# Optimization experiments

Measured on AMD Instinct MI355X. Metric: run time of the kernel, lower is better.

The kernel has to match this reference:

```python
import jax, jax.numpy as jnp
import numpy as np

N = 100_000      # nodes
E = 1_600_000    # edges (avg degree 16)
D = 128          # emb_dim
L = 2            # num_layer
BN_EPS = 1e-5


def setup_inputs() -> dict:
    key = jax.random.key(0)
    ks = jax.random.split(key, 16)
    s = 0.05
    inp = {
        # int inputs
        "x": jax.random.randint(ks[0], (N, 9), 0, 2),
        "z": jax.random.randint(ks[1], (N,), 0, 1000),
        "edge_index": jax.random.randint(ks[2], (2, E), 0, N),
        "edge_attr": jax.random.randint(ks[3], (E, 3), 0, 2),
        # learned params
        "atom_emb": jax.random.normal(ks[4], (9, 119, D), jnp.float32) * s,  # padded stacked AtomEncoder tables
        "z_emb": jax.random.normal(ks[5], (1000, D), jnp.float32) * s,
        "bond_emb": jax.random.normal(ks[6], (L, 3, 6, D), jnp.float32) * s,  # padded BondEncoder tables per layer
        "eps": jnp.zeros((L,), jnp.float32),
        "W1": jax.random.normal(ks[7], (L, D, 2 * D), jnp.float32) * s,
        "b1": jnp.zeros((L, 2 * D), jnp.float32),
        "g1": jnp.ones((L, 2 * D), jnp.float32),
        "be1": jnp.zeros((L, 2 * D), jnp.float32),
        "W2": jax.random.normal(ks[8], (L, 2 * D, D), jnp.float32) * s,
        "b2": jnp.zeros((L, D), jnp.float32),
        "bng": jnp.ones((L, D), jnp.float32),
        "bnb": jnp.zeros((L, D), jnp.float32),
    }
    return inp


def _batchnorm(h, g, b):
    # training-mode BatchNorm1d: batch stats, biased variance
    m = h.mean(axis=0)
    v = h.var(axis=0)
    return (h - m) * jax.lax.rsqrt(v + BN_EPS) * g + b


def _multi_embed(tables, idx):
    # tables: [F, V, D], idx: [N, F] -> sum_f tables[f][idx[:, f]]  -> [N, D]
    return jax.vmap(lambda t, i: t[i], in_axes=(0, 1))(tables, idx).sum(axis=0)


def reference(x, z, edge_index, edge_attr, atom_emb, z_emb, bond_emb, eps,
              W1, b1, g1, be1, W2, b2, bng, bnb):
    src, dst = edge_index[0], edge_index[1]
    # h0 = AtomEncoder(x) + z_embedding(z)
    h = _multi_embed(atom_emb, x) + z_emb[z]
    for l in range(L):
        # GINConv: bond encode -> gather -> relu message -> scatter-add -> MLP
        e_emb = _multi_embed(bond_emb[l], edge_attr)          # [E, D]
        msg = jax.nn.relu(h[src] + e_emb)                      # [E, D]
        agg = jax.ops.segment_sum(msg, dst, num_segments=N)    # [N, D]
        pre = (1.0 + eps[l]) * h + agg
        hid = jax.nn.relu(_batchnorm(pre @ W1[l] + b1[l], g1[l], be1[l]))
        hconv = hid @ W2[l] + b2[l]
        h = _batchnorm(hconv, bng[l], bnb[l])
        if l < L - 1:
            h = jax.nn.relu(h)   # dropout ratio 0 -> identity
    return h
```

## Files before the change

### kernel.cpp

```cpp
#include <hip/hip_runtime.h>

#define D 128
#define BN_EPS 1e-5f
#define NSUB 1024
#define CAP2 2048

typedef __attribute__((ext_vector_type(8))) short short8;
typedef __attribute__((ext_vector_type(4))) float floatx4;

__device__ __forceinline__ float bf2f(unsigned short u) {
    unsigned int x = ((unsigned int)u) << 16;
    return __builtin_bit_cast(float, x);
}
__device__ __forceinline__ unsigned short f2bf(float f) {
    unsigned int x = __builtin_bit_cast(unsigned int, f);
    x = x + 0x7FFFu + ((x >> 16) & 1u);
    return (unsigned short)(x >> 16);
}
__device__ __forceinline__ int magdiv(unsigned int x, unsigned long long magic) {
    return (int)(((unsigned long long)x * magic) >> 44);
}

__global__ __launch_bounds__(256)
void setup_kernel(const int* __restrict__ x, const int* __restrict__ z,
                  const float* __restrict__ atom_emb, const float* __restrict__ z_emb,
                  unsigned short* __restrict__ hb, int N, int nbNode,
                  const float* __restrict__ bond_emb, unsigned short* __restrict__ comb,
                  const float* __restrict__ W1, unsigned short* __restrict__ w1p,
                  const float* __restrict__ W2, unsigned short* __restrict__ w2p) {
    const int b = blockIdx.x;
    const int tid = threadIdx.x;
    if (b < nbNode) {
        int gid = b * 256 + tid;
        int node = gid >> 5;
        if (node >= N) return;
        int d0 = (gid & 31) * 4;
        float4 acc = *(const float4*)(z_emb + (size_t)z[node] * D + d0);
#pragma unroll
        for (int f = 0; f < 9; ++f) {
            int v = x[node * 9 + f];
            const float4 t = *(const float4*)(atom_emb + (size_t)(f * 119 + v) * D + d0);
            acc.x += t.x; acc.y += t.y; acc.z += t.z; acc.w += t.w;
        }
        ushort4 o;
        o.x = f2bf(acc.x); o.y = f2bf(acc.y); o.z = f2bf(acc.z); o.w = f2bf(acc.w);
        *(ushort4*)(hb + (size_t)node * D + d0) = o;
    } else if (b < nbNode + 216) {
        int t = (b - nbNode) * 256 + tid;
        int layer = t / (216 * D);
        int idx = t - layer * (216 * D);
        int c = idx >> 7, d = idx & 127;
        int a0 = c / 36, a1 = (c / 6) % 6, a2 = c % 6;
        const float* bb = bond_emb + (size_t)layer * 3 * 6 * D;
        float v = bb[(0 * 6 + a0) * D + d] + bb[(1 * 6 + a1) * D + d] + bb[(2 * 6 + a2) * D + d];
        comb[(size_t)layer * 216 * D + idx] = f2bf(v);
    } else {
        int isW2 = (b >= nbNode + 216 + 256);
        int t = (b - nbNode - 216 - (isW2 ? 256 : 0)) * 256 + tid;
        int layer = t >> 15;
        int idx = t & 32767;
        int logN = isW2 ? 7 : 8;
        int NCOLS = 1 << logN;
        int k = idx >> logN, n = idx & (NCOLS - 1);
        int k0 = k >> 5, kq = k & 31, q = kq >> 3, j = kq & 7;
        int tt = n >> 4, ln = n & 15;
        size_t dest = (((size_t)k0 * (NCOLS >> 4) + tt) << 9) + ((q << 4) + ln) * 8 + j;
        const float* W = (isW2 ? W2 : W1) + (size_t)layer * 32768;
        unsigned short* Wp = (isW2 ? w2p : w1p) + (size_t)layer * 32768;
        Wp[dest] = f2bf(W[idx]);
    }
}

__global__ __launch_bounds__(256)
void partition1_kernel(const int* __restrict__ ei, const int* __restrict__ ea,
                       int2* __restrict__ l1, int* __restrict__ tail1,
                       int E, unsigned long long magic, int capE, int ntiles, int nblocks) {
    __shared__ int lcnt[4][8], lbase[4][8];
    const int tid = threadIdx.x;
    const int wid = tid >> 6;
    for (int tile = blockIdx.x; tile < ntiles; tile += nblocks) {
        const int tb = tile * 4096;
        if (tid < 32) ((int*)lcnt)[tid] = 0;
        __syncthreads();
        int mydst[16], mypay[16];
#pragma unroll
        for (int j = 0; j < 16; ++j) {
            int e = tb + j * 256 + tid;
            if (e < E) {
                int dst = ei[E + e];
                int c = (ea[3 * e] * 6 + ea[3 * e + 1]) * 6 + ea[3 * e + 2];
                mydst[j] = dst;
                mypay[j] = ei[e] | (c << 17);
                atomicAdd(&lcnt[wid][magdiv((unsigned)dst * 8u, magic)], 1);
            } else {
                mydst[j] = -1;
            }
        }
        __syncthreads();
        if (tid < 32) {
            int w = tid >> 3, s = tid & 7;
            lbase[w][s] = atomicAdd(&tail1[s], lcnt[w][s]);
            lcnt[w][s] = 0;
        }
        __syncthreads();
#pragma unroll
        for (int j = 0; j < 16; ++j) {
            if (mydst[j] >= 0) {
                int s = magdiv((unsigned)mydst[j] * 8u, magic);
                int pos = lbase[wid][s] + atomicAdd(&lcnt[wid][s], 1);
                if (pos < capE) l1[(size_t)s * capE + pos] = make_int2(mydst[j], mypay[j]);
            }
        }
        __syncthreads();
    }
}

__global__ __launch_bounds__(256)
void partition2_kernel(const int2* __restrict__ l1, const int* __restrict__ tail1,
                       unsigned int* __restrict__ subL, int* __restrict__ tail2,
                       int N, unsigned long long magic, int capE, int G) {
    __shared__ int lcnt[128], lbase[128];
    const int s = blockIdx.x & 7;
    const int g = blockIdx.x >> 3;
    const int tid = threadIdx.x;
    const int len = min(tail1[s], capE);
    const int2* src = l1 + (size_t)s * capE;
    for (int tb = g * 4096; tb < len; tb += G * 4096) {
        if (tid < 128) lcnt[tid] = 0;
        __syncthreads();
        int2 e[16];
        int sub[16];
#pragma unroll
        for (int j = 0; j < 16; ++j) {
            int i = tb + j * 256 + tid;
            if (i < len) {
                e[j] = src[i];
                sub[j] = magdiv((unsigned)e[j].x * 1024u, magic) - (s << 7);
                atomicAdd(&lcnt[sub[j]], 1);
            } else {
                sub[j] = -1;
            }
        }
        __syncthreads();
        if (tid < 128) {
            lbase[tid] = atomicAdd(&tail2[(s << 7) + tid], lcnt[tid]);
            lcnt[tid] = 0;
        }
        __syncthreads();
#pragma unroll
        for (int j = 0; j < 16; ++j) {
            if (sub[j] >= 0) {
                int k = (s << 7) + sub[j];
                int lo = (int)(((long long)k * N + 1023) >> 10);
                int pos = lbase[sub[j]] + atomicAdd(&lcnt[sub[j]], 1);
                if (pos < CAP2)
                    subL[(size_t)k * CAP2 + pos] =
                        (unsigned int)e[j].y | ((unsigned int)(e[j].x - lo) << 25);
            }
        }
        __syncthreads();
    }
}

__global__ __launch_bounds__(1024)
void subscan_kernel(const int* __restrict__ tail2, int* __restrict__ subbase,
                    int* __restrict__ offsets, int N) {
    const int tid = threadIdx.x, lane = tid & 63, wid = tid >> 6;
    int v = min(tail2[tid], CAP2);
    int s = v;
#pragma unroll
    for (int off = 1; off < 64; off <<= 1) {
        int t = __shfl_up(s, off, 64);
        if (lane >= off) s += t;
    }
    __shared__ int ws[16];
    if (lane == 63) ws[wid] = s;
    __syncthreads();
    if (wid == 0) {
        int w = (lane < 16) ? ws[lane] : 0;
#pragma unroll
        for (int off = 1; off < 16; off <<= 1) {
            int t = __shfl_up(w, off, 64);
            if (lane >= off) w += t;
        }
        if (lane < 16) ws[lane] = w;
    }
    __syncthreads();
    int excl = (wid ? ws[wid - 1] : 0) + s - v;
    subbase[tid] = excl;
    if (tid == 1023) offsets[N] = excl + v;
}

__global__ __launch_bounds__(256)
void csr_sort_kernel(const unsigned int* __restrict__ subL, const int* __restrict__ tail2,
                     const int* __restrict__ subbase, int* __restrict__ offsets,
                     int* __restrict__ bucket, int N) {
    const int k = blockIdx.x;
    const int tid = threadIdx.x, lane = tid & 63, wid = tid >> 6;
    const int len = min(tail2[k], CAP2);
    const int base = subbase[k];
    const int lo = (int)(((long long)k * N + 1023) >> 10);
    const int hi = (int)(((long long)(k + 1) * N + 1023) >> 10);
    const int nn = hi - lo;
    __shared__ int cnt[128], loff[128], wsum[4];
    __shared__ unsigned int sorted[CAP2];
    const unsigned int* src = subL + (size_t)k * CAP2;

    if (tid < 128) cnt[tid] = 0;
    __syncthreads();
    for (int i = tid; i < len; i += 256) atomicAdd(&cnt[src[i] >> 25], 1);
    __syncthreads();
    int v = (tid < 128) ? cnt[tid] : 0;
    int s = v;
#pragma unroll
    for (int off = 1; off < 64; off <<= 1) {
        int t = __shfl_up(s, off, 64);
        if (lane >= off) s += t;
    }
    if (lane == 63) wsum[wid] = s;
    __syncthreads();
    if (tid < 128) loff[tid] = ((wid == 1) ? wsum[0] : 0) + s - v;
    __syncthreads();
    if (tid < nn) offsets[lo + tid] = base + loff[tid];
    if (tid < 128) cnt[tid] = 0;
    __syncthreads();
    for (int i = tid; i < len; i += 256) {
        unsigned int e = src[i];
        int ld = e >> 25;
        int pos = loff[ld] + atomicAdd(&cnt[ld], 1);
        sorted[pos] = e & 0x1FFFFFFu;
    }
    __syncthreads();
    for (int i = tid; i < len; i += 256) bucket[base + i] = (int)sorted[i];
}

__global__ __launch_bounds__(256)
void gather_reduce_kernel(const int* __restrict__ offsets, const int* __restrict__ bucket,
                          const unsigned short* __restrict__ comb,
                          const unsigned short* __restrict__ hb,
                          const float* __restrict__ eps_l,
                          unsigned short* __restrict__ pre, int N) {
    int gid = blockIdx.x * blockDim.x + threadIdx.x;
    int node = gid >> 4;
    if (node >= N) return;
    int d0 = (gid & 15) * 8;

    union U8 { int4 i; unsigned short u[8]; };
    float s = 1.0f + eps_l[0];
    float a[8];
    {
        U8 hv; hv.i = *(const int4*)(hb + (size_t)node * D + d0);
#pragma unroll
        for (int j = 0; j < 8; ++j) a[j] = bf2f(hv.u[j]) * s;
    }
    const int beg = offsets[node], end = offsets[node + 1];
    for (int p = beg; p < end; p += 4) {
        int rem = end - p;
        int pk0 = bucket[p];
        int pk1 = bucket[rem > 1 ? p + 1 : p];
        int pk2 = bucket[rem > 2 ? p + 2 : p];
        int pk3 = bucket[rem > 3 ? p + 3 : p];
        U8 h0, h1, h2, h3, c0, c1, c2, c3;
        h0.i = *(const int4*)(hb + (size_t)(pk0 & 0x1FFFF) * D + d0);
        c0.i = *(const int4*)(comb + (size_t)((pk0 >> 17) & 0xFF) * D + d0);
        h1.i = *(const int4*)(hb + (size_t)(pk1 & 0x1FFFF) * D + d0);
        c1.i = *(const int4*)(comb + (size_t)((pk1 >> 17) & 0xFF) * D + d0);
        h2.i = *(const int4*)(hb + (size_t)(pk2 & 0x1FFFF) * D + d0);
        c2.i = *(const int4*)(comb + (size_t)((pk2 >> 17) & 0xFF) * D + d0);
        h3.i = *(const int4*)(hb + (size_t)(pk3 & 0x1FFFF) * D + d0);
        c3.i = *(const int4*)(comb + (size_t)((pk3 >> 17) & 0xFF) * D + d0);
#pragma unroll
        for (int j = 0; j < 8; ++j) a[j] += fmaxf(bf2f(h0.u[j]) + bf2f(c0.u[j]), 0.0f);
        if (rem > 1) {
#pragma unroll
            for (int j = 0; j < 8; ++j) a[j] += fmaxf(bf2f(h1.u[j]) + bf2f(c1.u[j]), 0.0f);
        }
        if (rem > 2) {
#pragma unroll
            for (int j = 0; j < 8; ++j) a[j] += fmaxf(bf2f(h2.u[j]) + bf2f(c2.u[j]), 0.0f);
        }
        if (rem > 3) {
#pragma unroll
            for (int j = 0; j < 8; ++j) a[j] += fmaxf(bf2f(h3.u[j]) + bf2f(c3.u[j]), 0.0f);
        }
    }
    U8 o;
#pragma unroll
    for (int j = 0; j < 8; ++j) o.u[j] = f2bf(a[j]);
    *(int4*)(pre + (size_t)node * D + d0) = o.i;
}

template <int K, int NCOLS, int TRANSFORM, int OUTBF>
__global__ __launch_bounds__(256)
void mfma_gemm_kernel(const unsigned short* __restrict__ A,
                      const unsigned short* __restrict__ Wp,
                      const float* __restrict__ bias,
                      const float* __restrict__ tscale, const float* __restrict__ tshift,
                      unsigned short* __restrict__ Cbf, float* __restrict__ Cf,
                      float* __restrict__ partial, int M) {
    constexpr int NT = NCOLS / 16;
    constexpr int NCHUNK = K / 32;
    constexpr int CPP = NCHUNK / 2;
    __shared__ unsigned short Ws[16384];
    __shared__ float red[NCOLS * 2];

    const int tid = threadIdx.x;
    const int wave = tid >> 6, lane = tid & 63;
    const int quad = lane >> 4, ln = lane & 15;
    const int m_base = blockIdx.x * 64 + wave * 16;
    int arow = m_base + ln;
    if (arow >= M) arow = M - 1;
    const int kq = quad * 8;

    int4 araw[NCHUNK];
#pragma unroll
    for (int c = 0; c < NCHUNK; ++c)
        araw[c] = *(const int4*)(A + (size_t)arow * K + c * 32 + kq);

    for (int i = tid; i < NCOLS * 2; i += 256) red[i] = 0.f;

    floatx4 acc[NT];
#pragma unroll
    for (int t = 0; t < NT; ++t) acc[t] = (floatx4){0.f, 0.f, 0.f, 0.f};

#pragma unroll
    for (int ph = 0; ph < 2; ++ph) {
        if (ph) __syncthreads();
#pragma unroll
        for (int i = 0; i < 16384; i += 2048)
            *(int4*)&Ws[i + tid * 8] = *(const int4*)&Wp[ph * 16384 + i + tid * 8];
        __syncthreads();
#pragma unroll
        for (int cc = 0; cc < CPP; ++cc) {
            const int c = ph * CPP + cc;
            short8 afrag;
            if constexpr (TRANSFORM) {
                union { int4 i; unsigned short u[8]; } raw;
                raw.i = araw[c];
                const int kb = c * 32 + kq;
                float4 sc0 = *(const float4*)(tscale + kb);
                float4 sc1 = *(const float4*)(tscale + kb + 4);
                float4 sh0 = *(const float4*)(tshift + kb);
                float4 sh1 = *(const float4*)(tshift + kb + 4);
                union { short8 v; unsigned short u[8]; } au;
                au.u[0] = f2bf(fmaxf(bf2f(raw.u[0]) * sc0.x + sh0.x, 0.f));
                au.u[1] = f2bf(fmaxf(bf2f(raw.u[1]) * sc0.y + sh0.y, 0.f));
                au.u[2] = f2bf(fmaxf(bf2f(raw.u[2]) * sc0.z + sh0.z, 0.f));
                au.u[3] = f2bf(fmaxf(bf2f(raw.u[3]) * sc0.w + sh0.w, 0.f));
                au.u[4] = f2bf(fmaxf(bf2f(raw.u[4]) * sc1.x + sh1.x, 0.f));
                au.u[5] = f2bf(fmaxf(bf2f(raw.u[5]) * sc1.y + sh1.y, 0.f));
                au.u[6] = f2bf(fmaxf(bf2f(raw.u[6]) * sc1.z + sh1.z, 0.f));
                au.u[7] = f2bf(fmaxf(bf2f(raw.u[7]) * sc1.w + sh1.w, 0.f));
                afrag = au.v;
            } else {
                afrag = __builtin_bit_cast(short8, araw[c]);
            }
#pragma unroll
            for (int t = 0; t < NT; ++t) {
                short8 bfrag = *(const short8*)&Ws[(((cc * NT) + t) << 9) + lane * 8];
                acc[t] = __builtin_amdgcn_mfma_f32_16x16x32_bf16(afrag, bfrag, acc[t], 0, 0, 0);
            }
        }
    }

#pragma unroll
    for (int t = 0; t < NT; ++t) {
        int col = t * 16 + ln;
        float bv = bias[col];
        float sv = 0.f, qv = 0.f;
#pragma unroll
        for (int r = 0; r < 4; ++r) {
            int row = m_base + quad * 4 + r;
            if (row < M) {
                float v = acc[t][r] + bv;
                sv += v; qv += v * v;
                if constexpr (OUTBF) Cbf[(size_t)row * NCOLS + col] = f2bf(v);
                else                 Cf[(size_t)row * NCOLS + col] = v;
            }
        }
        sv += __shfl_xor(sv, 16, 64); sv += __shfl_xor(sv, 32, 64);
        qv += __shfl_xor(qv, 16, 64); qv += __shfl_xor(qv, 32, 64);
        if (quad == 0) {
            atomicAdd(&red[col], sv);
            atomicAdd(&red[NCOLS + col], qv);
        }
    }
    __syncthreads();
    float* pout = partial + (size_t)blockIdx.x * (NCOLS * 2);
    for (int i = tid; i < NCOLS * 2; i += 256) pout[i] = red[i];
}

template <int NCOLS>
__global__ __launch_bounds__(256)
void reduce_stats_kernel(const float* __restrict__ partial, int nb,
                         const float* __restrict__ g, const float* __restrict__ b,
                         float* __restrict__ scale, float* __restrict__ shift, float invN) {
    const int col = blockIdx.x;
    const int tid = threadIdx.x;
    float s = 0.f, q = 0.f;
    for (int bb = tid; bb < nb; bb += 256) {
        const float* p = partial + (size_t)bb * (NCOLS * 2);
        s += p[col];
        q += p[NCOLS + col];
    }
#pragma unroll
    for (int off = 32; off > 0; off >>= 1) {
        s += __shfl_xor(s, off, 64);
        q += __shfl_xor(q, off, 64);
    }
    __shared__ float ws[4], wq[4];
    if ((tid & 63) == 0) { ws[tid >> 6] = s; wq[tid >> 6] = q; }
    __syncthreads();
    if (tid == 0) {
        s = ws[0] + ws[1] + ws[2] + ws[3];
        q = wq[0] + wq[1] + wq[2] + wq[3];
        float mean = s * invN;
        float var = q * invN - mean * mean;
        float inv = 1.0f / sqrtf(var + BN_EPS);
        float sc = g[col] * inv;
        scale[col] = sc;
        shift[col] = b[col] - mean * sc;
    }
}

__global__ void bn_apply_kernel(const float* __restrict__ Xf, const unsigned short* __restrict__ Xb,
                                float* __restrict__ Yf, unsigned short* __restrict__ Yb,
                                const float* __restrict__ scale, const float* __restrict__ shift,
                                int N, int mode) {
    int gid = blockIdx.x * blockDim.x + threadIdx.x;
    int node = gid >> 5;
    if (node >= N) return;
    int d0 = (gid & 31) * 4;
    float4 v;
    if (mode == 0) {
        ushort4 b = *(const ushort4*)(Xb + (size_t)node * D + d0);
        v.x = bf2f(b.x); v.y = bf2f(b.y); v.z = bf2f(b.z); v.w = bf2f(b.w);
    } else {
        v = *(const float4*)(Xf + (size_t)node * D + d0);
    }
    float4 sc = *(const float4*)(scale + d0);
    float4 sh = *(const float4*)(shift + d0);
    float4 o;
    o.x = v.x * sc.x + sh.x;
    o.y = v.y * sc.y + sh.y;
    o.z = v.z * sc.z + sh.z;
    o.w = v.w * sc.w + sh.w;
    if (mode == 0) {
        ushort4 ob;
        ob.x = f2bf(fmaxf(o.x, 0.f));
        ob.y = f2bf(fmaxf(o.y, 0.f));
        ob.z = f2bf(fmaxf(o.z, 0.f));
        ob.w = f2bf(fmaxf(o.w, 0.f));
        *(ushort4*)(Yb + (size_t)node * D + d0) = ob;
    } else {
        *(float4*)(Yf + (size_t)node * D + d0) = o;
    }
}

extern "C" void kernel_launch(void* const* d_in, const int* in_sizes, int n_in,
                              void* d_out, int out_size, void* d_ws, size_t ws_size,
                              hipStream_t stream) {
    const int*   x        = (const int*)d_in[0];
    const int*   z        = (const int*)d_in[1];
    const int*   ei       = (const int*)d_in[2];
    const int*   ea       = (const int*)d_in[3];
    const float* atom_emb = (const float*)d_in[4];
    const float* z_emb    = (const float*)d_in[5];
    const float* bond_emb = (const float*)d_in[6];
    const float* eps      = (const float*)d_in[7];
    const float* W1       = (const float*)d_in[8];
    const float* b1       = (const float*)d_in[9];
    const float* g1       = (const float*)d_in[10];
    const float* be1      = (const float*)d_in[11];
    const float* W2       = (const float*)d_in[12];
    const float* b2       = (const float*)d_in[13];
    const float* bng      = (const float*)d_in[14];
    const float* bnb      = (const float*)d_in[15];

    const int N = in_sizes[1];
    const int E = in_sizes[3] / 3;

    float* h = (float*)d_out;

    const int ngb = (N + 63) / 64;
    const int capE = E / 8 + E / 64;
    const unsigned long long magic = ((1ULL << 44) / (unsigned int)N) + 1;

    char* ws = (char*)d_ws;
    size_t off = 0;
    auto alloc = [&](size_t bytes) { void* p = ws + off; off += (bytes + 255) & ~(size_t)255; return p; };
    unsigned short* pre_bf = (unsigned short*)alloc((size_t)N * D * 2);
    unsigned short* extra  = (unsigned short*)alloc((size_t)N * D * 2);
    (void)extra;
    float* out2 = (float*)pre_bf;
    unsigned short* out2_bf = pre_bf;
    unsigned short* out1_bf = (unsigned short*)alloc((size_t)N * 2 * D * 2);
    unsigned short* hb      = (unsigned short*)alloc((size_t)N * D * 2);
    int* offsets = (int*)alloc((size_t)(N + 1) * 4);
    int* bucket  = (int*)alloc((size_t)E * 4);
    int2* l1     = (int2*)alloc((size_t)8 * capE * 8);
    unsigned int* subL = (unsigned int*)alloc((size_t)NSUB * CAP2 * 4);
    int* subbase = (int*)alloc(NSUB * 4);
    float* stats = (float*)alloc(1024 * 4);
    float* partial1 = (float*)alloc((size_t)ngb * 512 * 4);
    float* partial2 = (float*)alloc((size_t)ngb * 256 * 4);
    unsigned short* w1p  = (unsigned short*)alloc((size_t)2 * D * 2 * D * 2);
    unsigned short* w2p  = (unsigned short*)alloc((size_t)2 * 2 * D * D * 2);
    unsigned short* comb = (unsigned short*)alloc((size_t)2 * 216 * D * 2);
    int* tail1 = (int*)out1_bf;
    int* tail2 = tail1 + 8;

    float* scale1 = stats;
    float* shift1 = stats + 256;
    float* scale2 = stats + 512;
    float* shift2 = stats + 640;

    const float invN = 1.0f / (float)N;
    const int ntiles = (E + 4095) / 4096;
    const int nbNode = (N * 32 + 255) / 256;

    hipMemsetAsync(tail1, 0, (8 + NSUB) * sizeof(int), stream);
    partition1_kernel<<<256, 256, 0, stream>>>(ei, ea, l1, tail1, E, magic, capE, ntiles, 256);
    partition2_kernel<<<256, 256, 0, stream>>>(l1, tail1, subL, tail2, N, magic, capE, 32);
    subscan_kernel<<<1, 1024, 0, stream>>>(tail2, subbase, offsets, N);
    csr_sort_kernel<<<NSUB, 256, 0, stream>>>(subL, tail2, subbase, offsets, bucket, N);

    setup_kernel<<<nbNode + 216 + 256 + 256, 256, 0, stream>>>(
        x, z, atom_emb, z_emb, hb, N, nbNode, bond_emb, comb, W1, w1p, W2, w2p);

    for (int l = 0; l < 2; ++l) {
        gather_reduce_kernel<<<(N * 16 + 255) / 256, 256, 0, stream>>>(
            offsets, bucket, comb + (size_t)l * 216 * D, hb, eps + l, pre_bf, N);

        mfma_gemm_kernel<128, 256, 0, 1><<<ngb, 256, 0, stream>>>(
            pre_bf, w1p + (size_t)l * D * 2 * D, b1 + (size_t)l * 2 * D,
            nullptr, nullptr, out1_bf, nullptr, partial1, N);
        reduce_stats_kernel<256><<<256, 256, 0, stream>>>(
            partial1, ngb, g1 + (size_t)l * 2 * D, be1 + (size_t)l * 2 * D,
            scale1, shift1, invN);

        if (l == 0) {
            mfma_gemm_kernel<256, 128, 1, 1><<<ngb, 256, 0, stream>>>(
                out1_bf, w2p + (size_t)l * 2 * D * D, b2 + (size_t)l * D,
                scale1, shift1, out2_bf, nullptr, partial2, N);
        } else {
            mfma_gemm_kernel<256, 128, 1, 0><<<ngb, 256, 0, stream>>>(
                out1_bf, w2p + (size_t)l * 2 * D * D, b2 + (size_t)l * D,
                scale1, shift1, nullptr, out2, partial2, N);
        }
        reduce_stats_kernel<128><<<128, 256, 0, stream>>>(
            partial2, ngb, bng + (size_t)l * D, bnb + (size_t)l * D,
            scale2, shift2, invN);

        bn_apply_kernel<<<(N * 32 + 255) / 256, 256, 0, stream>>>(
            out2, out2_bf, h, hb, scale2, shift2, N, l == 0 ? 0 : 1);
    }
}
```

Baseline: 574.7 us.

## Merge partition passes, widen gather to 64 lanes per node, drop fp32 output path

The two-stage edge partition becomes a single pass that bins edges straight into 1024 sub-buckets using shared counters, removing the intermediate l1 buffer and one kernel launch. The gather-reduce now gives each node a full 64-lane wavefront, with four edge groups in parallel and a shuffle reduction, so per-node latency on the irregular gathers shrinks. The last layer's second GEMM now writes bf16 instead of fp32 before BN apply, which cuts traffic but costs some output precision. Shared-memory atomics on 1024 counters may contend more, and idle lanes on low-degree nodes are a risk.

```diff
diff --git a/kernel.cpp b/kernel.cpp
--- a/kernel.cpp
+++ b/kernel.cpp
@@ -72,90 +72,49 @@
 }
 
 __global__ __launch_bounds__(256)
-void partition1_kernel(const int* __restrict__ ei, const int* __restrict__ ea,
-                       int2* __restrict__ l1, int* __restrict__ tail1,
-                       int E, unsigned long long magic, int capE, int ntiles, int nblocks) {
-    __shared__ int lcnt[4][8], lbase[4][8];
+void partition_kernel(const int* __restrict__ ei, const int* __restrict__ ea,
+                      unsigned int* __restrict__ subL, int* __restrict__ tail2,
+                      int E, int N, unsigned long long magic, int ntiles, int nblocks) {
+    __shared__ int lcnt[1024], lbase[1024];
     const int tid = threadIdx.x;
-    const int wid = tid >> 6;
     for (int tile = blockIdx.x; tile < ntiles; tile += nblocks) {
         const int tb = tile * 4096;
-        if (tid < 32) ((int*)lcnt)[tid] = 0;
+#pragma unroll
+        for (int i = 0; i < 4; ++i) lcnt[tid + i * 256] = 0;
         __syncthreads();
-        int mydst[16], mypay[16];
+        int sub[16];
+        unsigned int entry[16];
 #pragma unroll
         for (int j = 0; j < 16; ++j) {
             int e = tb + j * 256 + tid;
             if (e < E) {
                 int dst = ei[E + e];
                 int c = (ea[3 * e] * 6 + ea[3 * e + 1]) * 6 + ea[3 * e + 2];
-                mydst[j] = dst;
-                mypay[j] = ei[e] | (c << 17);
-                atomicAdd(&lcnt[wid][magdiv((unsigned)dst * 8u, magic)], 1);
-            } else {
-                mydst[j] = -1;
-            }
-        }
-        __syncthreads();
-        if (tid < 32) {
-            int w = tid >> 3, s = tid & 7;
-            lbase[w][s] = atomicAdd(&tail1[s], lcnt[w][s]);
-            lcnt[w][s] = 0;
-        }
-        __syncthreads();
-#pragma unroll
-        for (int j = 0; j < 16; ++j) {
-            if (mydst[j] >= 0) {
-                int s = magdiv((unsigned)mydst[j] * 8u, magic);
-                int pos = lbase[wid][s] + atomicAdd(&lcnt[wid][s], 1);
-                if (pos < capE) l1[(size_t)s * capE + pos] = make_int2(mydst[j], mypay[j]);
-            }
-        }
-        __syncthreads();
-    }
-}
-
-__global__ __launch_bounds__(256)
-void partition2_kernel(const int2* __restrict__ l1, const int* __restrict__ tail1,
-                       unsigned int* __restrict__ subL, int* __restrict__ tail2,
-                       int N, unsigned long long magic, int capE, int G) {
-    __shared__ int lcnt[128], lbase[128];
-    const int s = blockIdx.x & 7;
-    const int g = blockIdx.x >> 3;
-    const int tid = threadIdx.x;
-    const int len = min(tail1[s], capE);
-    const int2* src = l1 + (size_t)s * capE;
-    for (int tb = g * 4096; tb < len; tb += G * 4096) {
-        if (tid < 128) lcnt[tid] = 0;
-        __syncthreads();
-        int2 e[16];
-        int sub[16];
-#pragma unroll
-        for (int j = 0; j < 16; ++j) {
-            int i = tb + j * 256 + tid;
-            if (i < len) {
-                e[j] = src[i];
-                sub[j] = magdiv((unsigned)e[j].x * 1024u, magic) - (s << 7);
-                atomicAdd(&lcnt[sub[j]], 1);
+                int k = magdiv((unsigned)dst * 1024u, magic);
+                int lo = (int)(((long long)k * N + 1023) >> 10);
+                sub[j] = k;
+                entry[j] = (unsigned int)ei[e] | ((unsigned int)c << 17) |
+                           ((unsigned int)(dst - lo) << 25);
+                atomicAdd(&lcnt[k], 1);
             } else {
                 sub[j] = -1;
             }
         }
         __syncthreads();
-        if (tid < 128) {
-            lbase[tid] = atomicAdd(&tail2[(s << 7) + tid], lcnt[tid]);
-            lcnt[tid] = 0;
+#pragma unroll
+        for (int i = 0; i < 4; ++i) {
+            int k = tid + i * 256;
+            int c = lcnt[k];
+            if (c) lbase[k] = atomicAdd(&tail2[k], c);
+            lcnt[k] = 0;
         }
         __syncthreads();
 #pragma unroll
         for (int j = 0; j < 16; ++j) {
             if (sub[j] >= 0) {
-                int k = (s << 7) + sub[j];
-                int lo = (int)(((long long)k * N + 1023) >> 10);
-                int pos = lbase[sub[j]] + atomicAdd(&lcnt[sub[j]], 1);
-                if (pos < CAP2)
-                    subL[(size_t)k * CAP2 + pos] =
-                        (unsigned int)e[j].y | ((unsigned int)(e[j].x - lo) << 25);
+                int k = sub[j];
+                int pos = lbase[k] + atomicAdd(&lcnt[k], 1);
+                if (pos < CAP2) subL[(size_t)k * CAP2 + pos] = entry[j];
             }
         }
         __syncthreads();
@@ -240,54 +199,51 @@
                           const unsigned short* __restrict__ hb,
                           const float* __restrict__ eps_l,
                           unsigned short* __restrict__ pre, int N) {
-    int gid = blockIdx.x * blockDim.x + threadIdx.x;
-    int node = gid >> 4;
+    const int node = (blockIdx.x * 256 + threadIdx.x) >> 6;
     if (node >= N) return;
-    int d0 = (gid & 15) * 8;
+    const int lane = threadIdx.x & 63;
+    const int q = lane >> 4, ln = lane & 15;
+    const int d0 = ln * 8;
 
     union U8 { int4 i; unsigned short u[8]; };
-    float s = 1.0f + eps_l[0];
+    const int beg = offsets[node], end = offsets[node + 1];
+
     float a[8];
-    {
+#pragma unroll
+    for (int j = 0; j < 8; ++j) a[j] = 0.f;
+
+    for (int base = beg; base < end; base += 8) {
+        int e0 = base + q;
+        int e1 = base + 4 + q;
+        int pk0 = bucket[min(e0, end - 1)];
+        int pk1 = bucket[min(e1, end - 1)];
+        U8 h0, c0, h1, c1;
+        h0.i = *(const int4*)(hb + (size_t)(pk0 & 0x1FFFF) * D + d0);
+        c0.i = *(const int4*)(comb + (size_t)(pk0 >> 17) * D + d0);
+        h1.i = *(const int4*)(hb + (size_t)(pk1 & 0x1FFFF) * D + d0);
+        c1.i = *(const int4*)(comb + (size_t)(pk1 >> 17) * D + d0);
+        if (e0 < end) {
+#pragma unroll
+            for (int j = 0; j < 8; ++j) a[j] += fmaxf(bf2f(h0.u[j]) + bf2f(c0.u[j]), 0.0f);
+        }
+        if (e1 < end) {
+#pragma unroll
+            for (int j = 0; j < 8; ++j) a[j] += fmaxf(bf2f(h1.u[j]) + bf2f(c1.u[j]), 0.0f);
+        }
+    }
+#pragma unroll
+    for (int j = 0; j < 8; ++j) {
+        a[j] += __shfl_xor(a[j], 16, 64);
+        a[j] += __shfl_xor(a[j], 32, 64);
+    }
+    if (q == 0) {
+        const float s = 1.0f + eps_l[0];
         U8 hv; hv.i = *(const int4*)(hb + (size_t)node * D + d0);
-#pragma unroll
-        for (int j = 0; j < 8; ++j) a[j] = bf2f(hv.u[j]) * s;
-    }
-    const int beg = offsets[node], end = offsets[node + 1];
-    for (int p = beg; p < end; p += 4) {
-        int rem = end - p;
-        int pk0 = bucket[p];
-        int pk1 = bucket[rem > 1 ? p + 1 : p];
-        int pk2 = bucket[rem > 2 ? p + 2 : p];
-        int pk3 = bucket[rem > 3 ? p + 3 : p];
-        U8 h0, h1, h2, h3, c0, c1, c2, c3;
-        h0.i = *(const int4*)(hb + (size_t)(pk0 & 0x1FFFF) * D + d0);
-        c0.i = *(const int4*)(comb + (size_t)((pk0 >> 17) & 0xFF) * D + d0);
-        h1.i = *(const int4*)(hb + (size_t)(pk1 & 0x1FFFF) * D + d0);
-        c1.i = *(const int4*)(comb + (size_t)((pk1 >> 17) & 0xFF) * D + d0);
-        h2.i = *(const int4*)(hb + (size_t)(pk2 & 0x1FFFF) * D + d0);
-        c2.i = *(const int4*)(comb + (size_t)((pk2 >> 17) & 0xFF) * D + d0);
-        h3.i = *(const int4*)(hb + (size_t)(pk3 & 0x1FFFF) * D + d0);
-        c3.i = *(const int4*)(comb + (size_t)((pk3 >> 17) & 0xFF) * D + d0);
-#pragma unroll
-        for (int j = 0; j < 8; ++j) a[j] += fmaxf(bf2f(h0.u[j]) + bf2f(c0.u[j]), 0.0f);
-        if (rem > 1) {
-#pragma unroll
-            for (int j = 0; j < 8; ++j) a[j] += fmaxf(bf2f(h1.u[j]) + bf2f(c1.u[j]), 0.0f);
-        }
-        if (rem > 2) {
-#pragma unroll
-            for (int j = 0; j < 8; ++j) a[j] += fmaxf(bf2f(h2.u[j]) + bf2f(c2.u[j]), 0.0f);
-        }
-        if (rem > 3) {
-#pragma unroll
-            for (int j = 0; j < 8; ++j) a[j] += fmaxf(bf2f(h3.u[j]) + bf2f(c3.u[j]), 0.0f);
-        }
-    }
-    U8 o;
-#pragma unroll
-    for (int j = 0; j < 8; ++j) o.u[j] = f2bf(a[j]);
-    *(int4*)(pre + (size_t)node * D + d0) = o.i;
+        U8 o;
+#pragma unroll
+        for (int j = 0; j < 8; ++j) o.u[j] = f2bf(a[j] + s * bf2f(hv.u[j]));
+        *(int4*)(pre + (size_t)node * D + d0) = o.i;
+    }
 }
 
 template <int K, int NCOLS, int TRANSFORM, int OUTBF>
@@ -423,7 +379,7 @@
     }
 }
 
-__global__ void bn_apply_kernel(const float* __restrict__ Xf, const unsigned short* __restrict__ Xb,
+__global__ void bn_apply_kernel(const unsigned short* __restrict__ Xb,
                                 float* __restrict__ Yf, unsigned short* __restrict__ Yb,
                                 const float* __restrict__ scale, const float* __restrict__ shift,
                                 int N, int mode) {
@@ -431,13 +387,9 @@
     int node = gid >> 5;
     if (node >= N) return;
     int d0 = (gid & 31) * 4;
+    ushort4 b = *(const ushort4*)(Xb + (size_t)node * D + d0);
     float4 v;
-    if (mode == 0) {
-        ushort4 b = *(const ushort4*)(Xb + (size_t)node * D + d0);
-        v.x = bf2f(b.x); v.y = bf2f(b.y); v.z = bf2f(b.z); v.w = bf2f(b.w);
-    } else {
-        v = *(const float4*)(Xf + (size_t)node * D + d0);
-    }
+    v.x = bf2f(b.x); v.y = bf2f(b.y); v.z = bf2f(b.z); v.w = bf2f(b.w);
     float4 sc = *(const float4*)(scale + d0);
     float4 sh = *(const float4*)(shift + d0);
     float4 o;
@@ -483,22 +435,17 @@
     float* h = (float*)d_out;
 
     const int ngb = (N + 63) / 64;
-    const int capE = E / 8 + E / 64;
     const unsigned long long magic = ((1ULL << 44) / (unsigned int)N) + 1;
 
     char* ws = (char*)d_ws;
     size_t off = 0;
     auto alloc = [&](size_t bytes) { void* p = ws + off; off += (bytes + 255) & ~(size_t)255; return p; };
     unsigned short* pre_bf = (unsigned short*)alloc((size_t)N * D * 2);
-    unsigned short* extra  = (unsigned short*)alloc((size_t)N * D * 2);
-    (void)extra;
-    float* out2 = (float*)pre_bf;
     unsigned short* out2_bf = pre_bf;
     unsigned short* out1_bf = (unsigned short*)alloc((size_t)N * 2 * D * 2);
     unsigned short* hb      = (unsigned short*)alloc((size_t)N * D * 2);
     int* offsets = (int*)alloc((size_t)(N + 1) * 4);
     int* bucket  = (int*)alloc((size_t)E * 4);
-    int2* l1     = (int2*)alloc((size_t)8 * capE * 8);
     unsigned int* subL = (unsigned int*)alloc((size_t)NSUB * CAP2 * 4);
     int* subbase = (int*)alloc(NSUB * 4);
     float* stats = (float*)alloc(1024 * 4);
@@ -507,8 +454,7 @@
     unsigned short* w1p  = (unsigned short*)alloc((size_t)2 * D * 2 * D * 2);
     unsigned short* w2p  = (unsigned short*)alloc((size_t)2 * 2 * D * D * 2);
     unsigned short* comb = (unsigned short*)alloc((size_t)2 * 216 * D * 2);
-    int* tail1 = (int*)out1_bf;
-    int* tail2 = tail1 + 8;
+    int* tail2 = (int*)out1_bf;
 
     float* scale1 = stats;
     float* shift1 = stats + 256;
@@ -519,9 +465,8 @@
     const int ntiles = (E + 4095) / 4096;
     const int nbNode = (N * 32 + 255) / 256;
 
-    hipMemsetAsync(tail1, 0, (8 + NSUB) * sizeof(int), stream);
-    partition1_kernel<<<256, 256, 0, stream>>>(ei, ea, l1, tail1, E, magic, capE, ntiles, 256);
-    partition2_kernel<<<256, 256, 0, stream>>>(l1, tail1, subL, tail2, N, magic, capE, 32);
+    hipMemsetAsync(tail2, 0, NSUB * sizeof(int), stream);
+    partition_kernel<<<256, 256, 0, stream>>>(ei, ea, subL, tail2, E, N, magic, ntiles, 256);
     subscan_kernel<<<1, 1024, 0, stream>>>(tail2, subbase, offsets, N);
     csr_sort_kernel<<<NSUB, 256, 0, stream>>>(subL, tail2, subbase, offsets, bucket, N);
 
@@ -529,7 +474,7 @@
         x, z, atom_emb, z_emb, hb, N, nbNode, bond_emb, comb, W1, w1p, W2, w2p);
 
     for (int l = 0; l < 2; ++l) {
-        gather_reduce_kernel<<<(N * 16 + 255) / 256, 256, 0, stream>>>(
+        gather_reduce_kernel<<<(N * 64 + 255) / 256, 256, 0, stream>>>(
             offsets, bucket, comb + (size_t)l * 216 * D, hb, eps + l, pre_bf, N);
 
         mfma_gemm_kernel<128, 256, 0, 1><<<ngb, 256, 0, stream>>>(
@@ -539,20 +484,14 @@
             partial1, ngb, g1 + (size_t)l * 2 * D, be1 + (size_t)l * 2 * D,
             scale1, shift1, invN);
 
-        if (l == 0) {
-            mfma_gemm_kernel<256, 128, 1, 1><<<ngb, 256, 0, stream>>>(
-                out1_bf, w2p + (size_t)l * 2 * D * D, b2 + (size_t)l * D,
-                scale1, shift1, out2_bf, nullptr, partial2, N);
-        } else {
-            mfma_gemm_kernel<256, 128, 1, 0><<<ngb, 256, 0, stream>>>(
-                out1_bf, w2p + (size_t)l * 2 * D * D, b2 + (size_t)l * D,
-                scale1, shift1, nullptr, out2, partial2, N);
-        }
+        mfma_gemm_kernel<256, 128, 1, 1><<<ngb, 256, 0, stream>>>(
+            out1_bf, w2p + (size_t)l * 2 * D * D, b2 + (size_t)l * D,
+            scale1, shift1, out2_bf, nullptr, partial2, N);
         reduce_stats_kernel<128><<<128, 256, 0, stream>>>(
             partial2, ngb, bng + (size_t)l * D, bnb + (size_t)l * D,
             scale2, shift2, invN);
 
         bn_apply_kernel<<<(N * 32 + 255) / 256, 256, 0, stream>>>(
-            out2, out2_bf, h, hb, scale2, shift2, N, l == 0 ? 0 : 1);
-    }
-}
+            out2_bf, h, hb, scale2, shift2, N, l == 0 ? 0 : 1);
+    }
+}
```

Result: faster. 558.3 us (-2.9%).
